# Optimization experiments

Hardware: AMD Instinct MI355X
Metric: run time of the kernel (lower is better)

The kernel has to match this reference:

```python
import jax, jax.numpy as jnp
import numpy as np

N_PTS = 1048576
FEAT = 32
RES = 256


def _sample_plane(plane, gu, gv):
    """Bilinear grid_sample, align_corners=True.
    plane: (C, H, W); gu in [-1,1] indexes W, gv in [-1,1] indexes H.
    Returns (N, C)."""
    C, H, W = plane.shape
    px = (gu + 1.0) * 0.5 * (W - 1)
    py = (gv + 1.0) * 0.5 * (H - 1)
    x0 = jnp.floor(px)
    y0 = jnp.floor(py)
    wx = (px - x0)[None, :]
    wy = (py - y0)[None, :]
    x0i = jnp.clip(x0.astype(jnp.int32), 0, W - 1)
    x1i = jnp.clip(x0i + 1, 0, W - 1)
    y0i = jnp.clip(y0.astype(jnp.int32), 0, H - 1)
    y1i = jnp.clip(y0i + 1, 0, H - 1)
    f00 = plane[:, y0i, x0i]  # (C, N)
    f01 = plane[:, y0i, x1i]
    f10 = plane[:, y1i, x0i]
    f11 = plane[:, y1i, x1i]
    out = (f00 * (1 - wx) * (1 - wy) + f01 * wx * (1 - wy)
           + f10 * (1 - wx) * wy + f11 * wx * wy)
    return out.T  # (N, C)


def setup_inputs() -> dict:
    key = jax.random.key(0)
    ks = jax.random.split(key, 12)
    x = jax.random.uniform(ks[0], (N_PTS, 3), dtype=jnp.float32) * 2.0 - 0.5  # some outside box to exercise clamp
    d = jax.random.normal(ks[1], (N_PTS, 3), dtype=jnp.float32)
    plane_xy = jax.random.normal(ks[2], (FEAT, RES, RES), dtype=jnp.float32)
    plane_xz = jax.random.normal(ks[3], (FEAT, RES, RES), dtype=jnp.float32)
    plane_yz = jax.random.normal(ks[4], (FEAT, RES, RES), dtype=jnp.float32)
    center = jnp.zeros((3,), dtype=jnp.float32)
    scale = jnp.ones((3,), dtype=jnp.float32)
    s = 0.1
    w_sigma1 = jax.random.normal(ks[5], (3 * FEAT, 64), dtype=jnp.float32) * s
    w_sigma2 = jax.random.normal(ks[6], (64, 16), dtype=jnp.float32) * s
    w_color1 = jax.random.normal(ks[7], (15, 64), dtype=jnp.float32) * s
    w_color2 = jax.random.normal(ks[8], (64, 64), dtype=jnp.float32) * s
    w_color3 = jax.random.normal(ks[9], (64, 3), dtype=jnp.float32) * s
    return {"x": x, "d": d, "plane_xy": plane_xy, "plane_xz": plane_xz,
            "plane_yz": plane_yz, "center": center, "scale": scale,
            "w_sigma1": w_sigma1, "w_sigma2": w_sigma2,
            "w_color1": w_color1, "w_color2": w_color2, "w_color3": w_color3}


def reference(x, d, plane_xy, plane_xz, plane_yz, center, scale,
              w_sigma1, w_sigma2, w_color1, w_color2, w_color3):
    # normalize into unit cube and clamp
    xn = jnp.clip((x - center) / scale + 0.5, 0.0, 1.0)
    g = xn * 2.0 - 1.0  # (N, 3) in [-1, 1]
    gx, gy, gz = g[:, 0], g[:, 1], g[:, 2]
    # torch grid_sample: grid[...,0] indexes W (last dim), grid[...,1] indexes H
    feat_xy = _sample_plane(plane_xy, gx, gy)  # plane (C,resX,resY): W<-x, H<-y
    feat_xz = _sample_plane(plane_xz, gx, gz)
    feat_yz = _sample_plane(plane_yz, gy, gz)
    feat = jnp.concatenate([feat_xy, feat_xz, feat_yz], axis=1)  # (N, 96)
    # sigma net: 96 -> 64 (ReLU) -> 16, no bias (tcnn FullyFusedMLP)
    h = jax.nn.relu(feat @ w_sigma1)
    out16 = h @ w_sigma2  # (N, 16)
    sigma = out16[:, 0]
    # color net: 15 -> 64 -> 64 (ReLU) -> 3, sigmoid output
    c = jax.nn.relu(out16[:, 1:] @ w_color1)
    c = jax.nn.relu(c @ w_color2)
    color = jax.nn.sigmoid(c @ w_color3)
    return color, sigma
```

## Files before the change

kernel.cpp:

```cpp
#include <hip/hip_runtime.h>
#include <stdint.h>

typedef __attribute__((ext_vector_type(8))) unsigned short ushort8v;
typedef __attribute__((ext_vector_type(8))) short bf16x8;
typedef __attribute__((ext_vector_type(4))) float f32x4;
typedef __attribute__((ext_vector_type(2))) float f32x2;
typedef __attribute__((ext_vector_type(4))) unsigned int uint4v;

__device__ __forceinline__ float bf2f(unsigned short u) {
    return __uint_as_float(((unsigned)u) << 16);
}
__device__ __forceinline__ unsigned short f2bf(float f) {
    unsigned u = __float_as_uint(f);
    unsigned r = u + 0x7fffu + ((u >> 16) & 1u);
    return (unsigned short)(r >> 16);
}
__device__ __forceinline__ unsigned cvt_pk_bf16(float lo, float hi) {
    unsigned r;
    asm("v_cvt_pk_bf16_f32 %0, %1, %2" : "=v"(r) : "v"(lo), "v"(hi));
    return r;
}
__device__ __forceinline__ f32x2 up2(unsigned u) {
    f32x2 r;
    r[0] = __uint_as_float(u << 16);
    r[1] = __uint_as_float(u & 0xffff0000u);
    return r;
}

__global__ __launch_bounds__(256) void transpose_planes_kernel(
    const float* __restrict__ pxy, const float* __restrict__ pxz,
    const float* __restrict__ pyz, unsigned int* __restrict__ tp)
{
    __shared__ unsigned int lt[64 * 17];
    const int bid = blockIdx.x;
    const int plane = bid >> 10;
    const int base = (bid & 1023) * 64;
    const float* __restrict__ src = plane == 0 ? pxy : (plane == 1 ? pxz : pyz);
    const int tid = threadIdx.x;
    {
        const int c2 = tid >> 4;
        const int s  = tid & 15;
        const f32x4 va = *(const f32x4*)(src + (size_t)(2 * c2)     * 65536 + base + 4 * s);
        const f32x4 vb = *(const f32x4*)(src + (size_t)(2 * c2 + 1) * 65536 + base + 4 * s);
        #pragma unroll
        for (int j = 0; j < 4; ++j) {
            int yx = 4 * s + j;
            lt[yx * 17 + c2] = ((unsigned)f2bf(vb[j]) << 16) | (unsigned)f2bf(va[j]);
        }
    }
    __syncthreads();
    {
        const int yx = tid >> 2, q = tid & 3;
        uint4v o;
        #pragma unroll
        for (int k = 0; k < 4; ++k) o[k] = lt[yx * 17 + 4 * q + k];
        *(uint4v*)(tp + ((size_t)plane * 65536 + base + yx) * 16 + 4 * q) = o;
    }
}

__global__ __launch_bounds__(256) void pack_weights_kernel(
    const float* __restrict__ w1, const float* __restrict__ w2,
    const float* __restrict__ wc1, const float* __restrict__ wc2,
    const float* __restrict__ wc3, unsigned int* __restrict__ pack)
{
    int t = blockIdx.x * 256 + threadIdx.x;
    if (t >= 28 * 64) return;
    int lane = t & 63, tile = t >> 6;
    int mat, mt, kc;
    if (tile < 12)      { mat = 0; kc = tile >> 2;        mt = tile & 3; }
    else if (tile < 14) { mat = 1; kc = tile - 12;        mt = 0; }
    else if (tile < 18) { mat = 2; kc = 0;                mt = tile - 14; }
    else if (tile < 26) { mat = 3; kc = (tile - 18) >> 2; mt = (tile - 18) & 3; }
    else                { mat = 4; kc = tile - 26;        mt = 0; }
    int of = mt * 16 + (lane & 15);
    int kb = kc * 32 + (lane >> 4) * 8;
    float f[8];
    #pragma unroll
    for (int j = 0; j < 8; ++j) {
        int k = kb + j;
        float v;
        if (mat == 0)      v = w1[k * 64 + of];
        else if (mat == 1) v = w2[k * 16 + of];
        else if (mat == 2) v = (k >= 1 && k < 16) ? wc1[(k - 1) * 64 + of] : 0.0f;
        else if (mat == 3) v = wc2[k * 64 + of];
        else               v = (of < 3) ? wc3[k * 3 + of] : 0.0f;
        f[j] = v;
    }
    int sl = lane ^ (lane >> 3);
    unsigned int* dst = pack + tile * 256 + sl * 4;
    #pragma unroll
    for (int w = 0; w < 4; ++w)
        dst[w] = ((unsigned)f2bf(f[2 * w + 1]) << 16) | (unsigned)f2bf(f[2 * w]);
}

__global__ __launch_bounds__(512, 4) void nerf_mfma_kernel(
    const float* __restrict__ xin,
    const unsigned short* __restrict__ tp,
    const unsigned int* __restrict__ wpack,
    const float* __restrict__ center, const float* __restrict__ scale,
    float* __restrict__ out, int npts, int nwt)
{
    __shared__ unsigned int wlds[28 * 256];
    const int tid = threadIdx.x;
    #pragma unroll 2
    for (int idx = tid; idx < 28 * 256; idx += 512) wlds[idx] = wpack[idx];
    __syncthreads();

    const int lane = tid & 63;
    const int wv   = tid >> 6;
    const int p    = lane & 15;
    const int G    = lane >> 4;
    const bool hi32 = (lane & 32) != 0;
    const int sl   = lane ^ (lane >> 3);
    const bf16x8* Af = (const bf16x8*)wlds;
    const char* tpB = (const char*)tp;

    const float ctr0 = center[0], ctr1 = center[1], ctr2 = center[2];
    const float sc0 = scale[0], sc1 = scale[1], sc2 = scale[2];

    auto repack64 = [&](const unsigned pk[4][2], int kc2) -> bf16x8 {
        uint4v bw;
        #pragma unroll
        for (int w = 0; w < 4; ++w) {
            int src = p + 16 * (2 * (G & 1) + (w >> 1));
            unsigned lo_ = (unsigned)__shfl((int)pk[2 * kc2][w & 1], src, 64);
            unsigned hi_ = (unsigned)__shfl((int)pk[2 * kc2 + 1][w & 1], src, 64);
            bw[w] = hi32 ? hi_ : lo_;
        }
        return __builtin_bit_cast(bf16x8, bw);
    };

    for (int wtb = blockIdx.x * 16; wtb < nwt; wtb += gridDim.x * 16) {
        asm volatile("" ::: "memory");
        const int wt0 = wtb + wv * 2;
        int gpt[2]; bool valid[2];
        float us[2][3], vs[2][3];
        #pragma unroll
        for (int u = 0; u < 2; ++u) {
            const int wt = wt0 + u;
            gpt[u] = wt * 16 + p;
            valid[u] = (wt < nwt) && (gpt[u] < npts);
            const int rp = valid[u] ? gpt[u] : (npts - 1);
            const float xv = xin[3 * rp + 0], yv = xin[3 * rp + 1], zv = xin[3 * rp + 2];
            auto norm1 = [&](float v, float c, float s) {
                float xn = fminf(fmaxf((v - c) / s + 0.5f, 0.0f), 1.0f);
                return xn * 2.0f - 1.0f;
            };
            const float gx = norm1(xv, ctr0, sc0);
            const float gy = norm1(yv, ctr1, sc1);
            const float gz = norm1(zv, ctr2, sc2);
            us[u][0] = gx; us[u][1] = gx; us[u][2] = gy;
            vs[u][0] = gy; vs[u][1] = gz; vs[u][2] = gz;
        }

        f32x4 acc1[2][4];
        #pragma unroll
        for (int u = 0; u < 2; ++u)
            #pragma unroll
            for (int mt = 0; mt < 4; ++mt) acc1[u][mt] = f32x4{0.f, 0.f, 0.f, 0.f};

        #pragma unroll
        for (int pl = 0; pl < 3; ++pl) {
            uint4v cv[2][4];
            float wq[2][4];
            #pragma unroll
            for (int u = 0; u < 2; ++u) {
                float pxf = (us[u][pl] + 1.0f) * 0.5f * 255.0f;
                float pyf = (vs[u][pl] + 1.0f) * 0.5f * 255.0f;
                int x0 = (int)pxf, y0 = (int)pyf;
                float wx = pxf - (float)x0, wy = pyf - (float)y0;
                wq[u][0] = (1.f - wx) * (1.f - wy); wq[u][1] = wx * (1.f - wy);
                wq[u][2] = (1.f - wx) * wy;         wq[u][3] = wx * wy;
                const char* b00 = tpB + (((pl << 16) + (y0 << 8) + x0) << 6) + (G << 4);
                cv[u][0] = *(const uint4v*)(b00);
                cv[u][1] = *(const uint4v*)(b00 + 64);
                cv[u][2] = *(const uint4v*)(b00 + 16384);
                cv[u][3] = *(const uint4v*)(b00 + 16384 + 64);
            }
            bf16x8 bfr[2];
            #pragma unroll
            for (int u = 0; u < 2; ++u) {
                const f32x2 W00 = {wq[u][0], wq[u][0]}, W01 = {wq[u][1], wq[u][1]};
                const f32x2 W10 = {wq[u][2], wq[u][2]}, W11 = {wq[u][3], wq[u][3]};
                uint4v bw;
                #pragma unroll
                for (int w = 0; w < 4; ++w) {
                    f32x2 a = up2(cv[u][0][w]) * W00 + up2(cv[u][1][w]) * W01
                            + up2(cv[u][2][w]) * W10 + up2(cv[u][3][w]) * W11;
                    bw[w] = cvt_pk_bf16(a[0], a[1]);
                }
                bfr[u] = __builtin_bit_cast(bf16x8, bw);
            }
            #pragma unroll
            for (int mt = 0; mt < 4; ++mt) {
                const bf16x8 frag = Af[(pl * 4 + mt) * 64 + sl];
                #pragma unroll
                for (int u = 0; u < 2; ++u)
                    acc1[u][mt] = __builtin_amdgcn_mfma_f32_16x16x32_bf16(
                        frag, bfr[u], acc1[u][mt], 0, 0, 0);
            }
        }

        unsigned pk1[2][4][2];
        #pragma unroll
        for (int u = 0; u < 2; ++u)
            #pragma unroll
            for (int mt = 0; mt < 4; ++mt) {
                pk1[u][mt][0] = cvt_pk_bf16(fmaxf(acc1[u][mt][0], 0.f), fmaxf(acc1[u][mt][1], 0.f));
                pk1[u][mt][1] = cvt_pk_bf16(fmaxf(acc1[u][mt][2], 0.f), fmaxf(acc1[u][mt][3], 0.f));
            }
        f32x4 acc2[2];
        #pragma unroll
        for (int u = 0; u < 2; ++u) acc2[u] = f32x4{0.f, 0.f, 0.f, 0.f};
        #pragma unroll
        for (int kc2 = 0; kc2 < 2; ++kc2) {
            bf16x8 b[2];
            #pragma unroll
            for (int u = 0; u < 2; ++u) b[u] = repack64(pk1[u], kc2);
            const bf16x8 frag = Af[(12 + kc2) * 64 + sl];
            #pragma unroll
            for (int u = 0; u < 2; ++u)
                acc2[u] = __builtin_amdgcn_mfma_f32_16x16x32_bf16(frag, b[u], acc2[u], 0, 0, 0);
        }
        #pragma unroll
        for (int u = 0; u < 2; ++u)
            if (valid[u] && lane < 16) out[(size_t)3 * npts + gpt[u]] = acc2[u][0];

        bf16x8 b3[2];
        #pragma unroll
        for (int u = 0; u < 2; ++u) {
            unsigned pk2[2];
            pk2[0] = cvt_pk_bf16(acc2[u][0], acc2[u][1]);
            pk2[1] = cvt_pk_bf16(acc2[u][2], acc2[u][3]);
            uint4v bw3;
            #pragma unroll
            for (int w = 0; w < 4; ++w) {
                int src = p + 16 * (2 * (G & 1) + (w >> 1));
                unsigned v = (unsigned)__shfl((int)pk2[w & 1], src, 64);
                bw3[w] = (G < 2) ? v : 0u;
            }
            b3[u] = __builtin_bit_cast(bf16x8, bw3);
        }
        f32x4 acc3[2][4];
        #pragma unroll
        for (int u = 0; u < 2; ++u)
            #pragma unroll
            for (int mt = 0; mt < 4; ++mt) acc3[u][mt] = f32x4{0.f, 0.f, 0.f, 0.f};
        #pragma unroll
        for (int mt = 0; mt < 4; ++mt) {
            const bf16x8 frag = Af[(14 + mt) * 64 + sl];
            #pragma unroll
            for (int u = 0; u < 2; ++u)
                acc3[u][mt] = __builtin_amdgcn_mfma_f32_16x16x32_bf16(frag, b3[u], acc3[u][mt], 0, 0, 0);
        }

        unsigned pk3[2][4][2];
        #pragma unroll
        for (int u = 0; u < 2; ++u)
            #pragma unroll
            for (int mt = 0; mt < 4; ++mt) {
                pk3[u][mt][0] = cvt_pk_bf16(fmaxf(acc3[u][mt][0], 0.f), fmaxf(acc3[u][mt][1], 0.f));
                pk3[u][mt][1] = cvt_pk_bf16(fmaxf(acc3[u][mt][2], 0.f), fmaxf(acc3[u][mt][3], 0.f));
            }
        f32x4 acc4[2][4];
        #pragma unroll
        for (int u = 0; u < 2; ++u)
            #pragma unroll
            for (int mt = 0; mt < 4; ++mt) acc4[u][mt] = f32x4{0.f, 0.f, 0.f, 0.f};
        #pragma unroll
        for (int kc2 = 0; kc2 < 2; ++kc2) {
            bf16x8 b[2];
            #pragma unroll
            for (int u = 0; u < 2; ++u) b[u] = repack64(pk3[u], kc2);
            #pragma unroll
            for (int mt = 0; mt < 4; ++mt) {
                const bf16x8 frag = Af[(18 + kc2 * 4 + mt) * 64 + sl];
                #pragma unroll
                for (int u = 0; u < 2; ++u)
                    acc4[u][mt] = __builtin_amdgcn_mfma_f32_16x16x32_bf16(frag, b[u], acc4[u][mt], 0, 0, 0);
            }
        }

        unsigned pk4[2][4][2];
        #pragma unroll
        for (int u = 0; u < 2; ++u)
            #pragma unroll
            for (int mt = 0; mt < 4; ++mt) {
                pk4[u][mt][0] = cvt_pk_bf16(fmaxf(acc4[u][mt][0], 0.f), fmaxf(acc4[u][mt][1], 0.f));
                pk4[u][mt][1] = cvt_pk_bf16(fmaxf(acc4[u][mt][2], 0.f), fmaxf(acc4[u][mt][3], 0.f));
            }
        f32x4 acc5[2];
        #pragma unroll
        for (int u = 0; u < 2; ++u) acc5[u] = f32x4{0.f, 0.f, 0.f, 0.f};
        #pragma unroll
        for (int kc2 = 0; kc2 < 2; ++kc2) {
            bf16x8 b[2];
            #pragma unroll
            for (int u = 0; u < 2; ++u) b[u] = repack64(pk4[u], kc2);
            const bf16x8 frag = Af[(26 + kc2) * 64 + sl];
            #pragma unroll
            for (int u = 0; u < 2; ++u)
                acc5[u] = __builtin_amdgcn_mfma_f32_16x16x32_bf16(frag, b[u], acc5[u], 0, 0, 0);
        }
        #pragma unroll
        for (int u = 0; u < 2; ++u)
            if (valid[u] && lane < 16) {
                out[(size_t)3 * gpt[u] + 0] = 1.0f / (1.0f + __expf(-acc5[u][0]));
                out[(size_t)3 * gpt[u] + 1] = 1.0f / (1.0f + __expf(-acc5[u][1]));
                out[(size_t)3 * gpt[u] + 2] = 1.0f / (1.0f + __expf(-acc5[u][2]));
            }
    }
}

__global__ __launch_bounds__(256) void nerf_fallback_kernel(
    const float* __restrict__ xin,
    const float* __restrict__ pxy, const float* __restrict__ pxz,
    const float* __restrict__ pyz,
    const float* __restrict__ center, const float* __restrict__ scale,
    const float* __restrict__ w1, const float* __restrict__ w2,
    const float* __restrict__ wc1, const float* __restrict__ wc2,
    const float* __restrict__ wc3, float* __restrict__ out, int npts)
{
    __shared__ unsigned short act[64][256];
    const int tid = threadIdx.x;
    const int i = blockIdx.x * 256 + tid;
    if (i >= npts) return;
    const float xv = xin[3 * i], yv = xin[3 * i + 1], zv = xin[3 * i + 2];
    auto norm1 = [&](float v, int k) {
        float xn = fminf(fmaxf((v - center[k]) / scale[k] + 0.5f, 0.0f), 1.0f);
        return xn * 2.0f - 1.0f;
    };
    const float gx = norm1(xv, 0), gy = norm1(yv, 1), gz = norm1(zv, 2);
    float h[64];
    #pragma unroll
    for (int j = 0; j < 64; ++j) h[j] = 0.0f;
    auto samp = [&](float gu, float gv, int pl, const float* __restrict__ splane) {
        float pxf = (gu + 1.0f) * 0.5f * 255.0f, pyf = (gv + 1.0f) * 0.5f * 255.0f;
        float x0f = floorf(pxf), y0f = floorf(pyf);
        float wx = pxf - x0f, wy = pyf - y0f;
        int x0 = min(max((int)x0f, 0), 255), y0 = min(max((int)y0f, 0), 255);
        int x1 = min(x0 + 1, 255), y1 = min(y0 + 1, 255);
        float w00 = (1 - wx) * (1 - wy), w01 = wx * (1 - wy), w10 = (1 - wx) * wy, w11 = wx * wy;
        for (int c = 0; c < 32; ++c) {
            const float* b = splane + (size_t)c * 65536;
            float f = b[y0 * 256 + x0] * w00 + b[y0 * 256 + x1] * w01
                    + b[y1 * 256 + x0] * w10 + b[y1 * 256 + x1] * w11;
            const float* wr = w1 + (size_t)((pl * 32 + c) * 64);
            #pragma unroll
            for (int j = 0; j < 64; ++j) h[j] = fmaf(f, wr[j], h[j]);
        }
    };
    samp(gx, gy, 0, pxy); samp(gx, gz, 1, pxz); samp(gy, gz, 2, pyz);
    #pragma unroll
    for (int j = 0; j < 64; ++j) act[j][tid] = f2bf(fmaxf(h[j], 0.0f));
    float o[16];
    #pragma unroll
    for (int j = 0; j < 16; ++j) o[j] = 0.0f;
    for (int k = 0; k < 64; ++k) {
        float hv = bf2f(act[k][tid]);
        #pragma unroll
        for (int j = 0; j < 16; ++j) o[j] = fmaf(hv, w2[k * 16 + j], o[j]);
    }
    out[(size_t)3 * npts + i] = o[0];
    float c1[64];
    #pragma unroll
    for (int j = 0; j < 64; ++j) c1[j] = 0.0f;
    #pragma unroll
    for (int k = 0; k < 15; ++k)
        #pragma unroll
        for (int j = 0; j < 64; ++j) c1[j] = fmaf(o[k + 1], wc1[k * 64 + j], c1[j]);
    #pragma unroll
    for (int j = 0; j < 64; ++j) act[j][tid] = f2bf(fmaxf(c1[j], 0.0f));
    float c2[64];
    #pragma unroll
    for (int j = 0; j < 64; ++j) c2[j] = 0.0f;
    for (int k = 0; k < 64; ++k) {
        float v = bf2f(act[k][tid]);
        #pragma unroll
        for (int j = 0; j < 64; ++j) c2[j] = fmaf(v, wc2[k * 64 + j], c2[j]);
    }
    float r0 = 0, r1 = 0, r2 = 0;
    #pragma unroll
    for (int k = 0; k < 64; ++k) {
        float v = fmaxf(c2[k], 0.0f);
        r0 = fmaf(v, wc3[k * 3 + 0], r0);
        r1 = fmaf(v, wc3[k * 3 + 1], r1);
        r2 = fmaf(v, wc3[k * 3 + 2], r2);
    }
    out[(size_t)3 * i + 0] = 1.0f / (1.0f + expf(-r0));
    out[(size_t)3 * i + 1] = 1.0f / (1.0f + expf(-r1));
    out[(size_t)3 * i + 2] = 1.0f / (1.0f + expf(-r2));
}

extern "C" void kernel_launch(void* const* d_in, const int* in_sizes, int n_in,
                              void* d_out, int out_size, void* d_ws, size_t ws_size,
                              hipStream_t stream) {
    const float* x      = (const float*)d_in[0];
    const float* pxy    = (const float*)d_in[2];
    const float* pxz    = (const float*)d_in[3];
    const float* pyz    = (const float*)d_in[4];
    const float* center = (const float*)d_in[5];
    const float* scale  = (const float*)d_in[6];
    const float* w1     = (const float*)d_in[7];
    const float* w2     = (const float*)d_in[8];
    const float* wc1    = (const float*)d_in[9];
    const float* wc2    = (const float*)d_in[10];
    const float* wc3    = (const float*)d_in[11];
    float* out = (float*)d_out;
    const int npts = in_sizes[0] / 3;

    const size_t tp_bytes = (size_t)3 * 256 * 256 * 32 * 2;
    const size_t pack_bytes = 28 * 1024;
    if (ws_size >= tp_bytes + pack_bytes) {
        unsigned int* tp_ws   = (unsigned int*)d_ws;
        unsigned int* pack_ws = (unsigned int*)((char*)d_ws + tp_bytes);
        transpose_planes_kernel<<<3072, 256, 0, stream>>>(pxy, pxz, pyz, tp_ws);
        pack_weights_kernel<<<7, 256, 0, stream>>>(w1, w2, wc1, wc2, wc3, pack_ws);
        const int nwt = (npts + 15) / 16;
        nerf_mfma_kernel<<<1024, 512, 0, stream>>>(
            x, (const unsigned short*)tp_ws, pack_ws, center, scale, out, npts, nwt);
    } else {
        nerf_fallback_kernel<<<(npts + 255) / 256, 256, 0, stream>>>(
            x, pxy, pxz, pyz, center, scale, w1, w2, wc1, wc2, wc3, out, npts);
    }
}
```

Baseline: 192.1 us.

## Permute packed weight K-order so MFMA outputs feed next layer without shuffles

Reorders the K dimension of the packed weight fragments for the later layers (sigma2, color1/2/3), so each lane's accumulator outputs, once converted to bf16 pairs, directly form the B operand of the next MFMA. This removes the cross-lane shuffle repacking between layers. The launch-bounds occupancy hint is also relaxed, which may change register allocation. Correctness now depends on the permutation matching the accumulator layout exactly.

Result: faster. 186.2 us (-3.1%).

```diff
diff --git a/kernel.cpp b/kernel.cpp
--- a/kernel.cpp
+++ b/kernel.cpp
@@ -25,6 +25,10 @@
     r[0] = __uint_as_float(u << 16);
     r[1] = __uint_as_float(u & 0xffff0000u);
     return r;
+}
+__device__ __forceinline__ int pi64(int k) {
+    int G = (k >> 3) & 3, j = k & 7, kc2 = k >> 5;
+    return ((j >> 1) << 4) + (G << 2) + (j & 1) + (kc2 << 1);
 }
 
 __global__ __launch_bounds__(256) void transpose_planes_kernel(
@@ -80,10 +84,16 @@
         int k = kb + j;
         float v;
         if (mat == 0)      v = w1[k * 64 + of];
-        else if (mat == 1) v = w2[k * 16 + of];
-        else if (mat == 2) v = (k >= 1 && k < 16) ? wc1[(k - 1) * 64 + of] : 0.0f;
-        else if (mat == 3) v = wc2[k * 64 + of];
-        else               v = (of < 3) ? wc3[k * 3 + of] : 0.0f;
+        else if (mat == 1) v = w2[pi64(k) * 16 + of];
+        else if (mat == 2) {
+            int jj = k & 7, Gk = (k >> 3) & 3;
+            if (jj < 4) {
+                int ke = Gk * 4 + jj;
+                v = (ke >= 1) ? wc1[(ke - 1) * 64 + of] : 0.0f;
+            } else v = 0.0f;
+        }
+        else if (mat == 3) v = wc2[pi64(k) * 64 + of];
+        else               v = (of < 3) ? wc3[pi64(k) * 3 + of] : 0.0f;
         f[j] = v;
     }
     int sl = lane ^ (lane >> 3);
@@ -93,7 +103,7 @@
         dst[w] = ((unsigned)f2bf(f[2 * w + 1]) << 16) | (unsigned)f2bf(f[2 * w]);
 }
 
-__global__ __launch_bounds__(512, 4) void nerf_mfma_kernel(
+__global__ __launch_bounds__(512) void nerf_mfma_kernel(
     const float* __restrict__ xin,
     const unsigned short* __restrict__ tp,
     const unsigned int* __restrict__ wpack,
@@ -110,25 +120,12 @@
     const int wv   = tid >> 6;
     const int p    = lane & 15;
     const int G    = lane >> 4;
-    const bool hi32 = (lane & 32) != 0;
     const int sl   = lane ^ (lane >> 3);
     const bf16x8* Af = (const bf16x8*)wlds;
     const char* tpB = (const char*)tp;
 
     const float ctr0 = center[0], ctr1 = center[1], ctr2 = center[2];
     const float sc0 = scale[0], sc1 = scale[1], sc2 = scale[2];
-
-    auto repack64 = [&](const unsigned pk[4][2], int kc2) -> bf16x8 {
-        uint4v bw;
-        #pragma unroll
-        for (int w = 0; w < 4; ++w) {
-            int src = p + 16 * (2 * (G & 1) + (w >> 1));
-            unsigned lo_ = (unsigned)__shfl((int)pk[2 * kc2][w & 1], src, 64);
-            unsigned hi_ = (unsigned)__shfl((int)pk[2 * kc2 + 1][w & 1], src, 64);
-            bw[w] = hi32 ? hi_ : lo_;
-        }
-        return __builtin_bit_cast(bf16x8, bw);
-    };
 
     for (int wtb = blockIdx.x * 16; wtb < nwt; wtb += gridDim.x * 16) {
         asm volatile("" ::: "memory");
@@ -214,38 +211,30 @@
         for (int u = 0; u < 2; ++u) acc2[u] = f32x4{0.f, 0.f, 0.f, 0.f};
         #pragma unroll
         for (int kc2 = 0; kc2 < 2; ++kc2) {
-            bf16x8 b[2];
-            #pragma unroll
-            for (int u = 0; u < 2; ++u) b[u] = repack64(pk1[u], kc2);
             const bf16x8 frag = Af[(12 + kc2) * 64 + sl];
             #pragma unroll
-            for (int u = 0; u < 2; ++u)
-                acc2[u] = __builtin_amdgcn_mfma_f32_16x16x32_bf16(frag, b[u], acc2[u], 0, 0, 0);
+            for (int u = 0; u < 2; ++u) {
+                uint4v bw = {pk1[u][0][kc2], pk1[u][1][kc2], pk1[u][2][kc2], pk1[u][3][kc2]};
+                acc2[u] = __builtin_amdgcn_mfma_f32_16x16x32_bf16(
+                    frag, __builtin_bit_cast(bf16x8, bw), acc2[u], 0, 0, 0);
+            }
         }
         #pragma unroll
         for (int u = 0; u < 2; ++u)
             if (valid[u] && lane < 16) out[(size_t)3 * npts + gpt[u]] = acc2[u][0];
 
+        f32x4 acc3[2][4];
+        #pragma unroll
+        for (int u = 0; u < 2; ++u)
+            #pragma unroll
+            for (int mt = 0; mt < 4; ++mt) acc3[u][mt] = f32x4{0.f, 0.f, 0.f, 0.f};
         bf16x8 b3[2];
         #pragma unroll
         for (int u = 0; u < 2; ++u) {
-            unsigned pk2[2];
-            pk2[0] = cvt_pk_bf16(acc2[u][0], acc2[u][1]);
-            pk2[1] = cvt_pk_bf16(acc2[u][2], acc2[u][3]);
-            uint4v bw3;
-            #pragma unroll
-            for (int w = 0; w < 4; ++w) {
-                int src = p + 16 * (2 * (G & 1) + (w >> 1));
-                unsigned v = (unsigned)__shfl((int)pk2[w & 1], src, 64);
-                bw3[w] = (G < 2) ? v : 0u;
-            }
+            uint4v bw3 = {cvt_pk_bf16(acc2[u][0], acc2[u][1]),
+                          cvt_pk_bf16(acc2[u][2], acc2[u][3]), 0u, 0u};
             b3[u] = __builtin_bit_cast(bf16x8, bw3);
         }
-        f32x4 acc3[2][4];
-        #pragma unroll
-        for (int u = 0; u < 2; ++u)
-            #pragma unroll
-            for (int mt = 0; mt < 4; ++mt) acc3[u][mt] = f32x4{0.f, 0.f, 0.f, 0.f};
         #pragma unroll
         for (int mt = 0; mt < 4; ++mt) {
             const bf16x8 frag = Af[(14 + mt) * 64 + sl];
@@ -269,15 +258,15 @@
             for (int mt = 0; mt < 4; ++mt) acc4[u][mt] = f32x4{0.f, 0.f, 0.f, 0.f};
         #pragma unroll
         for (int kc2 = 0; kc2 < 2; ++kc2) {
-            bf16x8 b[2];
-            #pragma unroll
-            for (int u = 0; u < 2; ++u) b[u] = repack64(pk3[u], kc2);
             #pragma unroll
             for (int mt = 0; mt < 4; ++mt) {
                 const bf16x8 frag = Af[(18 + kc2 * 4 + mt) * 64 + sl];
                 #pragma unroll
-                for (int u = 0; u < 2; ++u)
-                    acc4[u][mt] = __builtin_amdgcn_mfma_f32_16x16x32_bf16(frag, b[u], acc4[u][mt], 0, 0, 0);
+                for (int u = 0; u < 2; ++u) {
+                    uint4v bw = {pk3[u][0][kc2], pk3[u][1][kc2], pk3[u][2][kc2], pk3[u][3][kc2]};
+                    acc4[u][mt] = __builtin_amdgcn_mfma_f32_16x16x32_bf16(
+                        frag, __builtin_bit_cast(bf16x8, bw), acc4[u][mt], 0, 0, 0);
+                }
             }
         }
 
@@ -294,13 +283,13 @@
         for (int u = 0; u < 2; ++u) acc5[u] = f32x4{0.f, 0.f, 0.f, 0.f};
         #pragma unroll
         for (int kc2 = 0; kc2 < 2; ++kc2) {
-            bf16x8 b[2];
-            #pragma unroll
-            for (int u = 0; u < 2; ++u) b[u] = repack64(pk4[u], kc2);
             const bf16x8 frag = Af[(26 + kc2) * 64 + sl];
             #pragma unroll
-            for (int u = 0; u < 2; ++u)
-                acc5[u] = __builtin_amdgcn_mfma_f32_16x16x32_bf16(frag, b[u], acc5[u], 0, 0, 0);
+            for (int u = 0; u < 2; ++u) {
+                uint4v bw = {pk4[u][0][kc2], pk4[u][1][kc2], pk4[u][2][kc2], pk4[u][3][kc2]};
+                acc5[u] = __builtin_amdgcn_mfma_f32_16x16x32_bf16(
+                    frag, __builtin_bit_cast(bf16x8, bw), acc5[u], 0, 0, 0);
+            }
         }
         #pragma unroll
         for (int u = 0; u < 2; ++u)
```
